# Kernel tuning notes

Measured on AMD Instinct MI355X. Metric: run time of the kernel, lower is better.

The kernel has to match this reference:

```python
import jax, jax.numpy as jnp
from jax import lax
import numpy as np

SIGNAL_DIM = 64
FR_SIZE = 4096
REG = 0.5
MAX_ITER = 25
TOL = 1e-5
BATCH = 1024


def make_dict():
    # D[t, f] = exp(i * 2*pi * f * t), f on grid [-0.5, 0.5) with spacing 1/FR_SIZE
    freq = jnp.arange(-0.5, 0.5, 1.0 / FR_SIZE, dtype=jnp.float32)[None, :]  # [1, F]
    t = jnp.arange(SIGNAL_DIM, dtype=jnp.float32)[:, None]                   # [N, 1]
    return jnp.exp(1j * 2.0 * jnp.pi * freq * t).astype(jnp.complex64)       # [N, F]


def setup_inputs() -> dict:
    key = jax.random.key(0)
    x = jax.random.normal(key, (BATCH, 2, SIGNAL_DIM), dtype=jnp.float32)
    return {"x": x, "D": make_dict()}


def _soft_complex(u, thr):
    # complex soft-threshold: shrink magnitude, keep phase
    mag = jnp.abs(u)
    scale = jnp.where(mag > thr, (mag - thr) / jnp.maximum(mag, 1e-12), 0.0)
    return u * scale.astype(u.dtype)


def reference(x, D):
    xc = (x[:, 0] + 1j * x[:, 1]).astype(jnp.complex64)  # [B, N]
    Dc = jnp.conj(D)                                      # [N, F]
    # D @ D^H = FR_SIZE * I for this oversampled Fourier dictionary,
    # so the Lipschitz constant of the gradient is L = sigma_max(D)^2 = FR_SIZE.
    step = jnp.float32(1.0 / FR_SIZE)
    thr = jnp.float32(REG) * step
    B = xc.shape[0]
    z0 = jnp.zeros((B, FR_SIZE), dtype=jnp.complex64)

    def cond(state):
        z, w, t, k, err = state
        return (k < MAX_ITER) & (err > TOL)

    def body(state):
        z, w, t, k, _ = state
        resid = w @ D.T - xc                 # [B, N]  (= (D z)^T - x)
        g = resid @ Dc                        # [B, F]  (= D^H resid)
        z_new = _soft_complex(w - step * g, thr)
        t_new = (1.0 + jnp.sqrt(1.0 + 4.0 * t * t)) / 2.0
        w_new = z_new + ((t - 1.0) / t_new).astype(jnp.complex64) * (z_new - z)
        err = jnp.linalg.norm(z_new - z) / jnp.maximum(jnp.linalg.norm(z), 1e-12)
        return (z_new, w_new, t_new, k + 1, err.astype(jnp.float32))

    init = (z0, z0, jnp.float32(1.0), jnp.int32(0), jnp.float32(jnp.inf))
    z_final, _, _, _, _ = lax.while_loop(cond, body, init)

    mag = jnp.abs(z_final)                    # [B, F]
    return mag / jnp.max(mag)                 # global-max normalization, as in torch .max()
```

## Files before the change

### kernel.cpp

```cpp
#include <hip/hip_runtime.h>
#include <math.h>

#define FR    4096
#define NSIG  64
#define NITER 25
#define BROWS 1024
#define PAD   258

typedef float v2f __attribute__((ext_vector_type(2)));

__device__ __forceinline__ v2f mk2(float a, float b) { v2f r; r.x = a; r.y = b; return r; }
__device__ __forceinline__ v2f sp(float a) { v2f r; r.x = a; r.y = a; return r; }

__device__ __forceinline__ v2f pk_add(v2f a, v2f b) {
    v2f d; asm("v_pk_add_f32 %0, %1, %2" : "=v"(d) : "v"(a), "v"(b)); return d;
}
__device__ __forceinline__ v2f pk_sub(v2f a, v2f b) {
    v2f d; asm("v_pk_add_f32 %0, %1, %2 neg_lo:[0,1] neg_hi:[0,1]" : "=v"(d) : "v"(a), "v"(b)); return d;
}
__device__ __forceinline__ v2f pk_addi(v2f a, v2f b) {
    v2f d; asm("v_pk_add_f32 %0, %1, %2 op_sel:[0,1] op_sel_hi:[1,0] neg_lo:[0,1] neg_hi:[0,0]"
               : "=v"(d) : "v"(a), "v"(b)); return d;
}
__device__ __forceinline__ v2f pk_subi(v2f a, v2f b) {
    v2f d; asm("v_pk_add_f32 %0, %1, %2 op_sel:[0,1] op_sel_hi:[1,0] neg_lo:[0,0] neg_hi:[0,1]"
               : "=v"(d) : "v"(a), "v"(b)); return d;
}
__device__ __forceinline__ v2f pk_fma_bl(v2f a, v2f b, v2f c) {
    v2f d;
    asm("v_pk_fma_f32 %0, %1, %2, %3 op_sel:[0,0,0] op_sel_hi:[0,1,1]"
        : "=v"(d) : "v"(a), "v"(b), "v"(c));
    return d;
}
__device__ __forceinline__ v2f pk_fmai_bh(v2f a, v2f b, v2f c) {
    v2f d;
    asm("v_pk_fma_f32 %0, %1, %2, %3 op_sel:[1,1,0] op_sel_hi:[1,0,1] neg_lo:[0,1,0]"
        : "=v"(d) : "v"(a), "v"(b), "v"(c));
    return d;
}
__device__ __forceinline__ v2f pk_muli_bh(v2f a, v2f b) {
    v2f d;
    asm("v_pk_mul_f32 %0, %1, %2 op_sel:[1,1] op_sel_hi:[1,0] neg_lo:[0,1]"
        : "=v"(d) : "v"(a), "v"(b));
    return d;
}
__device__ __forceinline__ v2f pk_mul_bl(v2f a, v2f b) {
    v2f d;
    asm("v_pk_mul_f32 %0, %1, %2 op_sel:[0,0] op_sel_hi:[0,1]"
        : "=v"(d) : "v"(a), "v"(b));
    return d;
}
__device__ __forceinline__ v2f cfma(v2f a, v2f b, v2f c) {
    return pk_fma_bl(a, b, pk_fmai_bh(a, b, c));
}
__device__ __forceinline__ v2f cmul(v2f a, v2f b) {
    return pk_fma_bl(a, b, pk_muli_bh(a, b));
}

__global__ void init_ws(unsigned* g) { *g = 0u; }

template<int S>
__device__ __forceinline__ void dft16p(v2f* X) {
    v2f s[4][4];
    #pragma unroll
    for (int r = 0; r < 4; ++r) {
        v2f a0 = X[r], a1 = X[r + 4], a2 = X[r + 8], a3 = X[r + 12];
        v2f b0 = pk_add(a0, a2), b1 = pk_sub(a0, a2);
        v2f b2 = pk_add(a1, a3), b3 = pk_sub(a1, a3);
        s[r][0] = pk_add(b0, b2);
        s[r][2] = pk_sub(b0, b2);
        if (S > 0) { s[r][1] = pk_addi(b1, b3); s[r][3] = pk_subi(b1, b3); }
        else       { s[r][1] = pk_subi(b1, b3); s[r][3] = pk_addi(b1, b3); }
    }
    const float C1 = 0.9238795325112867f;
    const float S1 = 0.3826834323650898f;
    const float H  = 0.7071067811865476f;
    const float sg = (S > 0) ? 1.0f : -1.0f;
    const v2f K1 = mk2(C1, sg * S1);
    const v2f KH = mk2(H,  sg * H);
    const v2f K3 = mk2(S1, sg * C1);
    #pragma unroll
    for (int p = 0; p < 4; ++p) {
        v2f t0 = s[0][p];
        v2f b0, b1, b2, b3;
        if (p == 0) {
            v2f t1 = s[1][0], t2 = s[2][0], t3 = s[3][0];
            b0 = pk_add(t0, t2); b1 = pk_sub(t0, t2);
            b2 = pk_add(t1, t3); b3 = pk_sub(t1, t3);
        } else if (p == 1) {
            v2f t1 = cmul(s[1][1], K1);
            v2f t2 = cmul(s[2][1], KH);
            v2f t3 = cmul(s[3][1], K3);
            b0 = pk_add(t0, t2); b1 = pk_sub(t0, t2);
            b2 = pk_add(t1, t3); b3 = pk_sub(t1, t3);
        } else if (p == 2) {
            v2f t1 = cmul(s[1][2], KH);
            v2f q3 = cmul(s[3][2], KH);
            if (S > 0) { b0 = pk_addi(t0, s[2][2]); b1 = pk_subi(t0, s[2][2]);
                         b2 = pk_addi(t1, q3);      b3 = pk_subi(t1, q3); }
            else       { b0 = pk_subi(t0, s[2][2]); b1 = pk_addi(t0, s[2][2]);
                         b2 = pk_subi(t1, q3);      b3 = pk_addi(t1, q3); }
        } else {
            v2f t1 = cmul(s[1][3], K3);
            v2f q2 = cmul(s[2][3], KH);
            v2f q3 = cmul(s[3][3], K1);
            if (S > 0) { b0 = pk_addi(t0, q2); b1 = pk_subi(t0, q2); }
            else       { b0 = pk_subi(t0, q2); b1 = pk_addi(t0, q2); }
            b2 = pk_sub(t1, q3); b3 = pk_add(t1, q3);
        }
        X[p]     = pk_add(b0, b2);
        X[p + 8] = pk_sub(b0, b2);
        if (S > 0) { X[p + 4] = pk_addi(b1, b3); X[p + 12] = pk_subi(b1, b3); }
        else       { X[p + 4] = pk_subi(b1, b3); X[p + 12] = pk_addi(b1, b3); }
    }
}

__global__ __launch_bounds__(256) void fista_kernel(const float* __restrict__ x,
                                                    float* __restrict__ out,
                                                    unsigned* __restrict__ gmax)
{
    __shared__ __attribute__((aligned(16))) v2f W_s[16 * PAD];
    __shared__ __attribute__((aligned(16))) v2f resid_s[NSIG];
    __shared__ v2f xc_s[NSIG];
    __shared__ v2f red_s[4][NSIG];
    __shared__ float wmax_s[4];

    const int tid  = (int)threadIdx.x;
    const int lane = tid & 63;
    const int wv   = tid >> 6;
    const int row  = (int)blockIdx.x;

    const float STEP = 1.0f / 4096.0f;
    const float THR  = 0.5f / 4096.0f;
    const float THR2 = THR * THR;

    if (tid < NSIG)
        xc_s[tid] = mk2(x[row * 128 + tid], x[row * 128 + 64 + tid]);

    v2f w[16], zo[16];
    #pragma unroll
    for (int k = 0; k < 16; ++k) { w[k] = sp(0.f); zo[k] = sp(0.f); }

    v2f P0, Rv, R2v, R4v, R8v;
    {
        float sn, cs;
        const float ang0 = (float)M_PI * (float)lane * (float)(wv - 32) * (1.0f / 32.0f);
        sincosf(ang0, &sn, &cs);                                      P0 = mk2(cs, sn);
        sincosf(2.0f * (float)M_PI * (float)lane * (1.0f / 4096.0f), &sn, &cs);
        Rv = mk2(cs, sn);
        R2v = cmul(Rv, Rv);
        R4v = cmul(R2v, R2v);
        R8v = cmul(R4v, R4v);
    }
    v2f Bv, B2v, B3v, Am[16];
    {
        const float td = (float)(tid - 2048);
        float sn, cs;
        v2f Av;
        sincosf(-2.0f * (float)M_PI * td * (1.0f / 4096.0f), &sn, &cs); Av = mk2(cs, sn);
        sincosf(-(float)M_PI * td * (1.0f / 128.0f), &sn, &cs);         Bv = mk2(cs, sn);
        sincosf(-(float)M_PI * td * (1.0f / 64.0f), &sn, &cs);          B2v = mk2(cs, sn);
        sincosf(-3.0f * (float)M_PI * td * (1.0f / 128.0f), &sn, &cs);  B3v = mk2(cs, sn);
        Am[0] = mk2(1.f, 0.f);
        #pragma unroll
        for (int m = 1; m < 16; ++m) Am[m] = cmul(Am[m - 1], Av);
    }

    float tf = 1.0f;

    for (int it = 0; it < NITER; ++it) {
        v2f X[16];
        #pragma unroll
        for (int k = 0; k < 16; ++k) X[k] = w[k];
        dft16p<1>(X);
        #pragma unroll
        for (int m = 0; m < 16; ++m)
            W_s[m * PAD + tid] = X[m];
        __syncthreads();

        {
            v2f acc0 = sp(0.f), acc1 = sp(0.f);
            v2f P = P0;
            const float4* W4 = (const float4*)W_s;
            const int base4 = ((lane & 15) * PAD + wv * 64) >> 1;
            #pragma unroll
            for (int c = 0; c < 8; ++c) {
                float4 a0 = W4[base4 + 4 * c + 0];
                float4 b0 = W4[base4 + 4 * c + 1];
                float4 a1 = W4[base4 + 4 * c + 2];
                float4 b1 = W4[base4 + 4 * c + 3];
                v2f pA = cfma(mk2(a0.z, a0.w), Rv, mk2(a0.x, a0.y));
                v2f pB = cfma(mk2(b0.z, b0.w), Rv, mk2(b0.x, b0.y));
                v2f Wc0 = cfma(pB, R2v, pA);
                acc0 = cfma(Wc0, P, acc0);
                v2f pC = cfma(mk2(a1.z, a1.w), Rv, mk2(a1.x, a1.y));
                v2f pD = cfma(mk2(b1.z, b1.w), Rv, mk2(b1.x, b1.y));
                v2f Wc1 = cfma(pD, R2v, pC);
                acc1 = cfma(Wc1, P, acc1);
                P = cmul(P, R8v);
            }
            red_s[wv][lane] = pk_add(acc0, cmul(acc1, R4v));
        }
        __syncthreads();
        if (tid < NSIG) {
            v2f r = pk_add(pk_add(red_s[0][tid], red_s[1][tid]),
                           pk_add(red_s[2][tid], red_s[3][tid]));
            resid_s[tid] = pk_sub(r, xc_s[tid]);
        }
        __syncthreads();

        v2f g[16];
        {
            const float4* r4 = (const float4*)resid_s;
            #pragma unroll
            for (int mp = 0; mp < 8; ++mp) {
                float4 q0 = r4[mp];
                float4 q1 = r4[mp + 8];
                float4 q2 = r4[mp + 16];
                float4 q3 = r4[mp + 24];
                #pragma unroll
                for (int h = 0; h < 2; ++h) {
                    v2f r0 = h ? mk2(q0.z, q0.w) : mk2(q0.x, q0.y);
                    v2f r1 = h ? mk2(q1.z, q1.w) : mk2(q1.x, q1.y);
                    v2f r2 = h ? mk2(q2.z, q2.w) : mk2(q2.x, q2.y);
                    v2f r3 = h ? mk2(q3.z, q3.w) : mk2(q3.x, q3.y);
                    v2f hA = cfma(r1, Bv, r0);
                    v2f hB = cfma(r3, B3v, cmul(r2, B2v));
                    g[2 * mp + h] = cmul(pk_add(hA, hB), Am[2 * mp + h]);
                }
            }
        }
        dft16p<-1>(g);

        float tn = 0.5f * (1.0f + sqrtf(fmaf(4.0f * tf, tf, 1.0f)));
        float mu = (tf - 1.0f) * __builtin_amdgcn_rcpf(tn);
        tf = tn;
        const v2f nstep = mk2(-STEP, 0.f);
        const v2f muv   = mk2(mu, 0.f);
        #pragma unroll
        for (int k = 0; k < 16; ++k) {
            v2f v = pk_fma_bl(nstep, g[k], w[k]);
            float m2 = fmaf(v.x, v.x, v.y * v.y);
            float q  = __builtin_amdgcn_rsqf(m2);
            float sc = (m2 * q - THR) * q;
            sc = (m2 > THR2) ? sc : 0.0f;
            v2f z = pk_mul_bl(mk2(sc, sc), v);
            v2f d = pk_sub(z, zo[k]);
            w[k] = pk_fma_bl(muv, d, z);
            zo[k] = z;
        }
    }

    float mg[16];
    float lmax = 0.f;
    #pragma unroll
    for (int k = 0; k < 16; ++k) {
        mg[k] = sqrtf(fmaf(zo[k].x, zo[k].x, zo[k].y * zo[k].y));
        lmax = fmaxf(lmax, mg[k]);
    }
    #pragma unroll
    for (int k = 0; k < 16; ++k)
        out[row * FR + k * 256 + tid] = mg[k];

    #pragma unroll
    for (int off = 32; off > 0; off >>= 1)
        lmax = fmaxf(lmax, __shfl_down(lmax, off));
    if (lane == 0) wmax_s[wv] = lmax;
    __syncthreads();
    if (tid == 0) {
        float m4 = fmaxf(fmaxf(wmax_s[0], wmax_s[1]), fmaxf(wmax_s[2], wmax_s[3]));
        atomicMax(gmax, __float_as_uint(m4));
    }
}

__global__ __launch_bounds__(256) void norm_kernel(float4* __restrict__ out,
                                                   const unsigned* __restrict__ gmax)
{
    const float inv = 1.0f / __uint_as_float(*gmax);
    int i = (int)blockIdx.x * 256 + (int)threadIdx.x;
    float4 v = out[i];
    v.x *= inv; v.y *= inv; v.z *= inv; v.w *= inv;
    out[i] = v;
}

extern "C" void kernel_launch(void* const* d_in, const int* in_sizes, int n_in,
                              void* d_out, int out_size, void* d_ws, size_t ws_size,
                              hipStream_t stream)
{
    const float* x = (const float*)d_in[0];
    float* out = (float*)d_out;
    unsigned* gmax = (unsigned*)d_ws;

    init_ws<<<1, 1, 0, stream>>>(gmax);
    fista_kernel<<<BROWS, 256, 0, stream>>>(x, out, gmax);
    norm_kernel<<<(FR * BROWS) / (256 * 4), 256, 0, stream>>>((float4*)out, gmax);
}
```

Baseline: 197.3 us.

## Replace cross-wave LDS residual reduction with wave-level shuffles and remap work

Remaps the residual computation so that each wave owns 16 output samples, with the four lane quarters splitting the frequency chunks. The partial sums are then reduced with xor-shuffles inside the wave instead of through a shared buffer, which removes one block barrier and the red_s buffer per iteration. To keep the new access pattern conflict-free, the LDS layout gets a different padding and per-wave index skew. The soft-threshold scale is also simplified to max(1 - thr*rsqrt(m2), 0), which changes behaviour when m2 is zero or denormal.

```diff
diff --git a/kernel.cpp b/kernel.cpp
--- a/kernel.cpp
+++ b/kernel.cpp
@@ -5,7 +5,7 @@
 #define NSIG  64
 #define NITER 25
 #define BROWS 1024
-#define PAD   258
+#define PADB  262
 
 typedef float v2f __attribute__((ext_vector_type(2)));
 
@@ -119,10 +119,9 @@
                                                     float* __restrict__ out,
                                                     unsigned* __restrict__ gmax)
 {
-    __shared__ __attribute__((aligned(16))) v2f W_s[16 * PAD];
+    __shared__ __attribute__((aligned(16))) v2f W_s[16 * PADB];
     __shared__ __attribute__((aligned(16))) v2f resid_s[NSIG];
     __shared__ v2f xc_s[NSIG];
-    __shared__ v2f red_s[4][NSIG];
     __shared__ float wmax_s[4];
 
     const int tid  = (int)threadIdx.x;
@@ -132,10 +131,14 @@
 
     const float STEP = 1.0f / 4096.0f;
     const float THR  = 0.5f / 4096.0f;
-    const float THR2 = THR * THR;
 
     if (tid < NSIG)
         xc_s[tid] = mk2(x[row * 128 + tid], x[row * 128 + 64 + tid]);
+
+    const int sidx = tid + 2 * (tid >> 6);
+
+    const int nB = 16 * wv + (lane & 15);
+    const int qB = lane >> 4;
 
     v2f w[16], zo[16];
     #pragma unroll
@@ -144,9 +147,9 @@
     v2f P0, Rv, R2v, R4v, R8v;
     {
         float sn, cs;
-        const float ang0 = (float)M_PI * (float)lane * (float)(wv - 32) * (1.0f / 32.0f);
+        const float ang0 = (float)M_PI * (float)nB * (float)(qB - 32) * (1.0f / 32.0f);
         sincosf(ang0, &sn, &cs);                                      P0 = mk2(cs, sn);
-        sincosf(2.0f * (float)M_PI * (float)lane * (1.0f / 4096.0f), &sn, &cs);
+        sincosf(2.0f * (float)M_PI * (float)nB * (1.0f / 4096.0f), &sn, &cs);
         Rv = mk2(cs, sn);
         R2v = cmul(Rv, Rv);
         R4v = cmul(R2v, R2v);
@@ -175,14 +178,14 @@
         dft16p<1>(X);
         #pragma unroll
         for (int m = 0; m < 16; ++m)
-            W_s[m * PAD + tid] = X[m];
+            W_s[m * PADB + sidx] = X[m];
         __syncthreads();
 
         {
             v2f acc0 = sp(0.f), acc1 = sp(0.f);
             v2f P = P0;
             const float4* W4 = (const float4*)W_s;
-            const int base4 = ((lane & 15) * PAD + wv * 64) >> 1;
+            const int base4 = 131 * (nB & 15) + 33 * qB;
             #pragma unroll
             for (int c = 0; c < 8; ++c) {
                 float4 a0 = W4[base4 + 4 * c + 0];
@@ -199,13 +202,14 @@
                 acc1 = cfma(Wc1, P, acc1);
                 P = cmul(P, R8v);
             }
-            red_s[wv][lane] = pk_add(acc0, cmul(acc1, R4v));
-        }
-        __syncthreads();
-        if (tid < NSIG) {
-            v2f r = pk_add(pk_add(red_s[0][tid], red_s[1][tid]),
-                           pk_add(red_s[2][tid], red_s[3][tid]));
-            resid_s[tid] = pk_sub(r, xc_s[tid]);
+            v2f part = pk_add(acc0, cmul(acc1, R4v));
+            v2f o;
+            o.x = __shfl_xor(part.x, 16); o.y = __shfl_xor(part.y, 16);
+            part = pk_add(part, o);
+            o.x = __shfl_xor(part.x, 32); o.y = __shfl_xor(part.y, 32);
+            part = pk_add(part, o);
+            if (qB == 0)
+                resid_s[nB] = pk_sub(part, xc_s[nB]);
         }
         __syncthreads();
 
@@ -242,8 +246,7 @@
             v2f v = pk_fma_bl(nstep, g[k], w[k]);
             float m2 = fmaf(v.x, v.x, v.y * v.y);
             float q  = __builtin_amdgcn_rsqf(m2);
-            float sc = (m2 * q - THR) * q;
-            sc = (m2 > THR2) ? sc : 0.0f;
+            float sc = fmaxf(fmaf(-THR, q, 1.0f), 0.0f);
             v2f z = pk_mul_bl(mk2(sc, sc), v);
             v2f d = pk_sub(z, zo[k]);
             w[k] = pk_fma_bl(muv, d, z);
```

New measurement: 199.9 us. About the same (+1.3%).

## Drop W_s barrier, compute residual redundantly per wave, simplify soft-threshold

Applied to the files above, without the earlier changes.

Each wave reads back only the W_s columns it wrote itself, so the barrier after the W_s store is removed. Every wave now sums the four partial reductions and subtracts x, keeping its own copy of the residual; this replaces the single-wave residual step and its idle threads. The soft-threshold is rewritten as max(1 - THR*rsq, 0), which drops the compare and select. The final block max also becomes one atomic per wave, which removes an end barrier in exchange for more global atomics.

```diff
diff --git a/kernel.cpp b/kernel.cpp
--- a/kernel.cpp
+++ b/kernel.cpp
@@ -120,10 +120,8 @@
                                                     unsigned* __restrict__ gmax)
 {
     __shared__ __attribute__((aligned(16))) v2f W_s[16 * PAD];
-    __shared__ __attribute__((aligned(16))) v2f resid_s[NSIG];
-    __shared__ v2f xc_s[NSIG];
-    __shared__ v2f red_s[4][NSIG];
-    __shared__ float wmax_s[4];
+    __shared__ __attribute__((aligned(16))) v2f red_s[4 * NSIG];
+    __shared__ __attribute__((aligned(16))) v2f resid_w[4 * NSIG];
 
     const int tid  = (int)threadIdx.x;
     const int lane = tid & 63;
@@ -132,10 +130,8 @@
 
     const float STEP = 1.0f / 4096.0f;
     const float THR  = 0.5f / 4096.0f;
-    const float THR2 = THR * THR;
-
-    if (tid < NSIG)
-        xc_s[tid] = mk2(x[row * 128 + tid], x[row * 128 + 64 + tid]);
+
+    const v2f xc_r = mk2(x[row * 128 + lane], x[row * 128 + 64 + lane]);
 
     v2f w[16], zo[16];
     #pragma unroll
@@ -176,7 +172,6 @@
         #pragma unroll
         for (int m = 0; m < 16; ++m)
             W_s[m * PAD + tid] = X[m];
-        __syncthreads();
 
         {
             v2f acc0 = sp(0.f), acc1 = sp(0.f);
@@ -199,19 +194,23 @@
                 acc1 = cfma(Wc1, P, acc1);
                 P = cmul(P, R8v);
             }
-            red_s[wv][lane] = pk_add(acc0, cmul(acc1, R4v));
+            red_s[wv * NSIG + lane] = pk_add(acc0, cmul(acc1, R4v));
         }
         __syncthreads();
-        if (tid < NSIG) {
-            v2f r = pk_add(pk_add(red_s[0][tid], red_s[1][tid]),
-                           pk_add(red_s[2][tid], red_s[3][tid]));
-            resid_s[tid] = pk_sub(r, xc_s[tid]);
+
+        {
+            v2f s0 = red_s[lane];
+            v2f s1 = red_s[NSIG + lane];
+            v2f s2 = red_s[2 * NSIG + lane];
+            v2f s3 = red_s[3 * NSIG + lane];
+            v2f r  = pk_sub(pk_add(pk_add(s0, s1), pk_add(s2, s3)), xc_r);
+            resid_w[wv * NSIG + lane] = r;
         }
         __syncthreads();
 
         v2f g[16];
         {
-            const float4* r4 = (const float4*)resid_s;
+            const float4* r4 = (const float4*)(resid_w + wv * NSIG);
             #pragma unroll
             for (int mp = 0; mp < 8; ++mp) {
                 float4 q0 = r4[mp];
@@ -242,8 +241,7 @@
             v2f v = pk_fma_bl(nstep, g[k], w[k]);
             float m2 = fmaf(v.x, v.x, v.y * v.y);
             float q  = __builtin_amdgcn_rsqf(m2);
-            float sc = (m2 * q - THR) * q;
-            sc = (m2 > THR2) ? sc : 0.0f;
+            float sc = fmaxf(fmaf(-THR, q, 1.0f), 0.0f);
             v2f z = pk_mul_bl(mk2(sc, sc), v);
             v2f d = pk_sub(z, zo[k]);
             w[k] = pk_fma_bl(muv, d, z);
@@ -265,12 +263,8 @@
     #pragma unroll
     for (int off = 32; off > 0; off >>= 1)
         lmax = fmaxf(lmax, __shfl_down(lmax, off));
-    if (lane == 0) wmax_s[wv] = lmax;
-    __syncthreads();
-    if (tid == 0) {
-        float m4 = fmaxf(fmaxf(wmax_s[0], wmax_s[1]), fmaxf(wmax_s[2], wmax_s[3]));
-        atomicMax(gmax, __float_as_uint(m4));
-    }
+    if (lane == 0)
+        atomicMax(gmax, __float_as_uint(lmax));
 }
 
 __global__ __launch_bounds__(256) void norm_kernel(float4* __restrict__ out,
```

Measured after the change: 202.4 us. +2.6%, slower.
